# Kernel tuning notes

Hardware: AMD Instinct MI355X
Metric: run time of the kernel (lower is better)

Reference implementation:

```python
import jax, jax.numpy as jnp
import numpy as np

HIDDEN = 256
HEADS = 8
HEAD_DIM = HIDDEN // HEADS  # 32
N_NODES = 50000
N_EDGES = 800000


def setup_inputs() -> dict:
    key = jax.random.key(0)
    ks = jax.random.split(key, 12)
    h = jax.random.normal(ks[0], (N_NODES, HIDDEN), dtype=jnp.float32)
    row = jax.random.randint(ks[1], (N_EDGES,), 0, N_NODES, dtype=jnp.int64 if jax.config.jax_enable_x64 else jnp.int32)
    col = jax.random.randint(ks[2], (N_EDGES,), 0, N_NODES, dtype=jnp.int64 if jax.config.jax_enable_x64 else jnp.int32)
    def lin(kw, kb):
        W = jax.random.normal(kw, (HIDDEN, HIDDEN), dtype=jnp.float32) * 0.02
        b = jax.random.normal(kb, (HIDDEN,), dtype=jnp.float32) * 0.02
        return W, b
    Wq, bq = lin(ks[3], ks[4])
    Wk, bk = lin(ks[5], ks[6])
    Wv, bv = lin(ks[7], ks[8])
    Wo, bo = lin(ks[9], ks[10])
    return {"h": h, "row": row, "col": col,
            "Wq": Wq, "bq": bq, "Wk": Wk, "bk": bk,
            "Wv": Wv, "bv": bv, "Wo": Wo, "bo": bo}


def reference(h, row, col, Wq, bq, Wk, bk, Wv, bv, Wo, bo):
    N = h.shape[0]
    scaling = HEAD_DIM ** (-0.5)
    # torch Linear: x @ W.T + b; reshape to (N, head_dim, num_heads) as in source
    q = (h @ Wq.T + bq).reshape(N, HEAD_DIM, HEADS) * scaling
    k = (h @ Wk.T + bk).reshape(N, HEAD_DIM, HEADS)
    v = (h @ Wv.T + bv).reshape(N, HEAD_DIM, HEADS)
    # SDDMM: per-edge, per-head score = q[row] . k[col]   -> [E, H]
    s = jnp.einsum('edh,edh->eh', q[row], k[col])
    # sparse softmax over nonzeros of each row
    m = jax.ops.segment_max(s, row, num_segments=N)          # [N, H]
    e = jnp.exp(s - m[row])                                   # [E, H]
    z = jax.ops.segment_sum(e, row, num_segments=N)          # [N, H]
    attn = e / z[row]                                         # [E, H]
    # SPMM: out[i] = sum over edges (i,j) attn[e,h] * v[j,:,h]
    out = jax.ops.segment_sum(attn[:, None, :] * v[col], row, num_segments=N)  # [N, D, H]
    return out.reshape(N, -1) @ Wo.T + bo
```

## Files before the change

kernel.cpp:

```cpp
#include <hip/hip_runtime.h>
#include <hip/hip_bf16.h>
#include <math.h>

#define N_NODES  50000
#define N_EDGES  800000
#define HIDDEN   256
#define HEADS    8
#define HEAD_DIM 32
#define MAXDEG   64
#define KVSTRIDE 512
#define QKV_NB   2346
#define O_NB     782

#define PREP_BKT   391
#define PREP_HCONV 6400
#define PREP_W     450
#define PREP_NB    (PREP_BKT + PREP_HCONV + PREP_W)

using short8 = __attribute__((ext_vector_type(8))) short;
using f32x4  = __attribute__((ext_vector_type(4))) float;

__device__ __forceinline__ float b2f(unsigned short u) {
  union { unsigned int i; float f; } v; v.i = ((unsigned int)u) << 16; return v.f;
}
__device__ __forceinline__ unsigned short f2b(float f) {
  union { float f; unsigned int i; } v; v.f = f;
  unsigned int r = v.i + 0x7FFF + ((v.i >> 16) & 1);
  return (unsigned short)(r >> 16);
}
__device__ __forceinline__ void unpack2(unsigned int d, float& lo, float& hi) {
  union { unsigned int i; float f; } a, b;
  a.i = d << 16; b.i = d & 0xFFFF0000u;
  lo = a.f; hi = b.f;
}

template<int NB, int NCT>
__device__ __forceinline__ void xcd_map(int b, int& rt, int& ct) {
  constexpr int q = NB / 8, r = NB % 8;
  const int xcd = b & 7, j = b >> 3;
  const int id = (xcd < r ? xcd * (q + 1) : r * (q + 1) + (xcd - r) * q) + j;
  rt = id / NCT; ct = id - rt * NCT;
}

__global__ __launch_bounds__(256) void init(const unsigned short* __restrict__ h16,
                                            const int* __restrict__ rowraw,
                                            int* __restrict__ flags,
                                            int* __restrict__ cur) {
  const int tid = threadIdx.x;
  if (blockIdx.x == 0) {
    __shared__ int nan_cnt, hi_viol, lo_pos;
    if (tid == 0) { nan_cnt = 0; hi_viol = 0; lo_pos = 0; }
    __syncthreads();
    int local = 0;
    for (int i = tid; i < 16384; i += 256)
      if ((h16[i] & 0x7F80) == 0x7F80) local++;
    if (local) atomicAdd(&nan_cnt, local);
    int viol = 0, pos = 0;
    for (int e = tid; e < 512; e += 256) {
      if (rowraw[2 * e + 1] != 0) viol++;
      if (rowraw[2 * e] > 0) pos++;
    }
    if (viol) atomicAdd(&hi_viol, viol);
    if (pos) atomicAdd(&lo_pos, pos);
    __syncthreads();
    if (tid == 0) {
      flags[0] = (nan_cnt >= 4) ? 1 : 0;
      flags[1] = (hi_viol == 0 && lo_pos > 0) ? 1 : 0;
    }
  } else {
    const int i = (blockIdx.x - 1) * 256 + tid;
    if (i < N_NODES / 4) ((int4*)cur)[i] = make_int4(0, 0, 0, 0);
  }
}

struct WPtrs {
  const void* srcW[4]; unsigned short* dstW[4];
  const void* srcB[4]; unsigned short* dstB[4];
};

__global__ __launch_bounds__(256) void prep(
    const void* __restrict__ hsrc, unsigned short* __restrict__ Hc, WPtrs p,
    const int* __restrict__ rowraw, const int* __restrict__ colraw,
    const int* __restrict__ flags, int* __restrict__ cursor,
    unsigned short* __restrict__ bucket)
{
  const int fp32 = flags[0];
  const int bid = blockIdx.x, tid = threadIdx.x;

  if (bid < PREP_BKT) {
    const int t = bid * 256 + tid;
    if (t < N_EDGES / 8) {
      const int i64 = flags[1];
      const int e0 = t * 8;
      int r[8], c[8];
      #pragma unroll
      for (int x = 0; x < 8; ++x) {
        const int e = e0 + x;
        r[x] = i64 ? rowraw[2 * e] : rowraw[e];
        c[x] = i64 ? colraw[2 * e] : colraw[e];
      }
      int pos[8];
      #pragma unroll
      for (int x = 0; x < 8; ++x)
        pos[x] = atomicAdd(&cursor[r[x]], 1);
      #pragma unroll
      for (int x = 0; x < 8; ++x)
        if (pos[x] < MAXDEG) bucket[r[x] * MAXDEG + pos[x]] = (unsigned short)c[x];
    }
  } else if (bid < PREP_BKT + PREP_HCONV) {
    const int n4 = N_NODES * HIDDEN / 4;
    for (int i = (bid - PREP_BKT) * 256 + tid; i < n4; i += PREP_HCONV * 256) {
      if (fp32) {
        const float4 v = ((const float4*)hsrc)[i];
        ushort4 o; o.x = f2b(v.x); o.y = f2b(v.y); o.z = f2b(v.z); o.w = f2b(v.w);
        ((ushort4*)Hc)[i] = o;
      } else {
        ((ushort4*)Hc)[i] = ((const ushort4*)hsrc)[i];
      }
    }
  } else {
    const int idx = (bid - PREP_BKT - PREP_HCONV) * 256 + tid;
    if (idx < 49152) {
      const int m = idx >> 14, r = idx & 16383;
      const int g = r >> 6, kc = r & 63;
      const int f = ((g & 31) << 3) | (g >> 5);
      const int s = f * 64 + kc;
      if (fp32) {
        const float4 v = ((const float4*)p.srcW[m])[s];
        ushort4 o; o.x = f2b(v.x); o.y = f2b(v.y); o.z = f2b(v.z); o.w = f2b(v.w);
        ((ushort4*)p.dstW[m])[g * 64 + kc] = o;
      } else {
        ((ushort4*)p.dstW[m])[g * 64 + kc] = ((const ushort4*)p.srcW[m])[s];
      }
    } else if (idx < 49152 + 65536) {
      const int g = idx - 49152;
      const int f = g >> 8, kk = g & 255;
      const int s = f * 256 + (((kk & 31) << 3) | (kk >> 5));
      p.dstW[3][g] = fp32 ? f2b(((const float*)p.srcW[3])[s])
                          : ((const unsigned short*)p.srcW[3])[s];
    } else if (idx < 49152 + 65536 + 256) {
      const int t = idx - 49152 - 65536;
      const int m = t >> 6, r = t & 63;
      if (m < 3) {
        ushort4 o;
        #pragma unroll
        for (int x = 0; x < 4; ++x) {
          const int g = r * 4 + x;
          const int f = ((g & 31) << 3) | (g >> 5);
          ((unsigned short*)&o)[x] = fp32 ? f2b(((const float*)p.srcB[m])[f])
                                          : ((const unsigned short*)p.srcB[m])[f];
        }
        ((ushort4*)p.dstB[m])[r] = o;
      } else {
        if (fp32) {
          const float4 v = ((const float4*)p.srcB[3])[r];
          ushort4 o; o.x = f2b(v.x); o.y = f2b(v.y); o.z = f2b(v.z); o.w = f2b(v.w);
          ((ushort4*)p.dstB[3])[r] = o;
        } else {
          ((ushort4*)p.dstB[3])[r] = ((const ushort4*)p.srcB[3])[r];
        }
      }
    }
  }
}

#if defined(__has_builtin)
#if __has_builtin(__builtin_amdgcn_global_load_lds)
#define HAVE_GLL 1
#endif
#endif
__device__ __forceinline__ void stage_tile(
    const unsigned short* __restrict__ src, int row_base, int row_max,
    int kb, unsigned short* lds, int wave, int lane)
{
  #pragma unroll
  for (int c = 0; c < 4; ++c) {
    const int chunk = wave * 4 + c;
    const int r = chunk * 8 + (lane >> 3);
    int gr = row_base + r; if (gr > row_max) gr = row_max;
    const int scb = (lane & 7) ^ ((lane >> 3) & 7);
    const unsigned short* gp = src + (size_t)gr * HIDDEN + kb * 64 + scb * 8;
#ifdef HAVE_GLL
    __builtin_amdgcn_global_load_lds(
        (const __attribute__((address_space(1))) void*)gp,
        (__attribute__((address_space(3))) void*)(lds + chunk * 512),
        16, 0, 0);
#else
    *(short8*)(lds + chunk * 512 + lane * 8) = *(const short8*)gp;
#endif
  }
}

#define GEMM_CORE(A_SRC, AROWB, AROWM, B_SRC, BROWB, BROWM)                          \
  __shared__ unsigned short sA[2][8192], sB[2][8192];                                \
  const int wave = threadIdx.x >> 6, lane = threadIdx.x & 63;                        \
  const int lrow = lane & 15, quad = lane >> 4;                                      \
  const int wr0 = (wave & 1) * 64, wc0 = (wave >> 1) * 64;                           \
  f32x4 acc[4][4];                                                                   \
  _Pragma("unroll")                                                                  \
  for (int i = 0; i < 4; ++i)                                                        \
    _Pragma("unroll")                                                                \
    for (int j = 0; j < 4; ++j) acc[i][j] = (f32x4){0.f, 0.f, 0.f, 0.f};            \
  stage_tile(A_SRC, AROWB, AROWM, 0, sA[0], wave, lane);                             \
  stage_tile(B_SRC, BROWB, BROWM, 0, sB[0], wave, lane);                             \
  _Pragma("unroll")                                                                  \
  for (int kb = 0; kb < 4; ++kb) {                                                   \
    __syncthreads();                          \
    if (kb < 3) {                                                                    \
      stage_tile(A_SRC, AROWB, AROWM, kb + 1, sA[(kb + 1) & 1], wave, lane);         \
      stage_tile(B_SRC, BROWB, BROWM, kb + 1, sB[(kb + 1) & 1], wave, lane);         \
    }                                                                                \
    const unsigned short* pA = sA[kb & 1];                                           \
    const unsigned short* pB = sB[kb & 1];                                           \
    _Pragma("unroll")                                                                \
    for (int kk = 0; kk < 2; ++kk) {                                                 \
      short8 af[4], bf[4];                                                           \
      _Pragma("unroll")                                                              \
      for (int i = 0; i < 4; ++i) {                                                  \
        const int rr = wr0 + i * 16 + lrow;                                          \
        af[i] = *(const short8*)(pA + rr * 64 + (((kk * 4 + quad) ^ (lrow & 7)) * 8));\
      }                                                                              \
      _Pragma("unroll")                                                              \
      for (int j = 0; j < 4; ++j) {                                                  \
        const int rr = wc0 + j * 16 + lrow;                                          \
        bf[j] = *(const short8*)(pB + rr * 64 + (((kk * 4 + quad) ^ (lrow & 7)) * 8));\
      }                                                                              \
      _Pragma("unroll")                                                              \
      for (int i = 0; i < 4; ++i)                                                    \
        _Pragma("unroll")                                                            \
        for (int j = 0; j < 4; ++j)                                                  \
          acc[i][j] = __builtin_amdgcn_mfma_f32_16x16x32_bf16(af[i], bf[j], acc[i][j], 0, 0, 0); \
    }                                                                                \
  }

__global__ __launch_bounds__(256) void gemm_qkv(
    const unsigned short* __restrict__ X, const unsigned short* __restrict__ WQKV,
    const unsigned short* __restrict__ biasAll,
    unsigned short* __restrict__ Qt, unsigned short* __restrict__ KV, float qscale)
{
  int rt, ct; xcd_map<QKV_NB, 6>(blockIdx.x, rt, ct);
  const int row0 = rt * 128;
  const int col0 = ct * 128;
  GEMM_CORE(X, row0, N_NODES - 1, WQKV, col0, 767)

  #pragma unroll
  for (int j = 0; j < 4; ++j) {
    const int gcol = col0 + wc0 + j * 16;
    const int m = gcol >> 8;
    const int f = (gcol & 255) + lrow;
    const float scale = (m == 0) ? qscale : 1.0f;
    const float bv = b2f(biasAll[gcol + lrow]);
    unsigned short* bp = (m == 0) ? Qt : (KV + ((m == 2) ? 256 : 0));
    const int ldv = (m == 0) ? 256 : KVSTRIDE;
    #pragma unroll
    for (int i = 0; i < 4; ++i) {
      #pragma unroll
      for (int r = 0; r < 4; ++r) {
        const int row = row0 + wr0 + i * 16 + quad * 4 + r;
        if (row < N_NODES)
          bp[(size_t)row * ldv + f] = f2b((acc[i][j][r] + bv) * scale);
      }
    }
  }
}

__global__ __launch_bounds__(256) void gemm_o(
    const unsigned short* __restrict__ X, const unsigned short* __restrict__ W,
    const unsigned short* __restrict__ bias, void* __restrict__ Yv,
    const int* __restrict__ flags)
{
  int rt, ct; xcd_map<O_NB, 2>(blockIdx.x, rt, ct);
  const int row0 = rt * 128;
  const int col0 = ct * 128;
  const int out_fp32 = flags[0];
  GEMM_CORE(X, row0, N_NODES - 1, W, col0, 255)

  #pragma unroll
  for (int j = 0; j < 4; ++j) {
    const int col = col0 + wc0 + j * 16 + lrow;
    const float bv = b2f(bias[col]);
    #pragma unroll
    for (int i = 0; i < 4; ++i) {
      #pragma unroll
      for (int r = 0; r < 4; ++r) {
        const int row = row0 + wr0 + i * 16 + quad * 4 + r;
        if (row < N_NODES) {
          const float y = acc[i][j][r] + bv;
          if (out_fp32) ((float*)Yv)[(size_t)row * HIDDEN + col] = y;
          else ((unsigned short*)Yv)[(size_t)row * HIDDEN + col] = f2b(y);
        }
      }
    }
  }
}

__global__ __launch_bounds__(256) void attn_fused(
    const unsigned short* __restrict__ Qt, const unsigned short* __restrict__ KV,
    const int* __restrict__ cursor, const unsigned short* __restrict__ bucket,
    unsigned short* __restrict__ pre)
{
  const int node = blockIdx.x * 4 + (threadIdx.x >> 6);
  if (node >= N_NODES) return;
  const int lane = threadIdx.x & 63;
  const int side = lane >> 5;
  const int sub  = lane & 31;
  const unsigned suboff = (unsigned)(sub * 8);
  int cnt = cursor[node]; if (cnt > MAXDEG) cnt = MAXDEG;

  const uint4 qd = *(const uint4*)(Qt + (unsigned)node * HIDDEN + suboff);
  float q[8];
  unpack2(qd.x, q[0], q[1]); unpack2(qd.y, q[2], q[3]);
  unpack2(qd.z, q[4], q[5]); unpack2(qd.w, q[6], q[7]);

  float a[8] = {0.f, 0.f, 0.f, 0.f, 0.f, 0.f, 0.f, 0.f};
  float z = 0.f;

  if (cnt > 0) {
    const int last = cnt - 1;
    const unsigned short* brow = bucket + node * MAXDEG;
    const int myidx = (int)brow[lane <= last ? lane : last];
    const int nit = (cnt + 1) >> 1;

    auto compute = [&](const uint4& kk, const uint4& vv, int jj) {
      float kf[8];
      unpack2(kk.x, kf[0], kf[1]); unpack2(kk.y, kf[2], kf[3]);
      unpack2(kk.z, kf[4], kf[5]); unpack2(kk.w, kf[6], kf[7]);
      float s0 = q[0]*kf[0] + q[2]*kf[2] + q[4]*kf[4] + q[6]*kf[6];
      float s1 = q[1]*kf[1] + q[3]*kf[3] + q[5]*kf[5] + q[7]*kf[7];
      float d = s0 + s1;
      d += __shfl_xor(d, 1, 64);
      d += __shfl_xor(d, 2, 64);
      float w = __expf(d);
      if (2 * jj + side > last) w = 0.f;
      z += w;
      float vf[8];
      unpack2(vv.x, vf[0], vf[1]); unpack2(vv.y, vf[2], vf[3]);
      unpack2(vv.z, vf[4], vf[5]); unpack2(vv.w, vf[6], vf[7]);
      #pragma unroll
      for (int x = 0; x < 8; ++x) a[x] = fmaf(w, vf[x], a[x]);
    };

    const int cA = __shfl(myidx, side, 64);
    const unsigned offA = ((unsigned)cA << 9) + suboff;
    uint4 kA = *(const uint4*)(KV + offA);
    uint4 vA = *(const uint4*)(KV + offA + 256u);

    const int cB = __shfl(myidx, 2 + side, 64);
    const unsigned offB = ((unsigned)cB << 9) + suboff;
    uint4 kB = *(const uint4*)(KV + offB);
    uint4 vB = *(const uint4*)(KV + offB + 256u);

    int slC = 4 + side;
    int cC = __shfl(myidx, slC, 64);

    int j = 0;
    #pragma unroll 2
    for (; j + 2 < nit; ++j) {
      const unsigned offC = ((unsigned)cC << 9) + suboff;
      const uint4 kC = *(const uint4*)(KV + offC);
      const uint4 vC = *(const uint4*)(KV + offC + 256u);
      int sl = 2 * (j + 3) + side; if (sl > 63) sl = 63;
      cC = __shfl(myidx, sl, 64);
      compute(kA, vA, j);
      kA = kB; vA = vB; kB = kC; vB = vC;
    }
    compute(kA, vA, j);
    if (j + 1 < nit) compute(kB, vB, j + 1);
  }

  #pragma unroll
  for (int x = 0; x < 8; ++x) a[x] += __shfl_xor(a[x], 32, 64);
  z += __shfl_xor(z, 32, 64);
  const float zi = (z > 0.f) ? (1.f / z) : 0.f;

  if (side == 0) {
    short8 ov;
    #pragma unroll
    for (int x = 0; x < 8; ++x) ov[x] = (short)f2b(a[x] * zi);
    *(short8*)(pre + (unsigned)node * HIDDEN + suboff) = ov;
  }
}

extern "C" void kernel_launch(void* const* d_in, const int* in_sizes, int n_in,
                              void* d_out, int out_size, void* d_ws, size_t ws_size,
                              hipStream_t stream) {
  const void* h_raw  = d_in[0];
  const int* row_raw = (const int*)d_in[1];
  const int* col_raw = (const int*)d_in[2];
  const void* Wq_raw = d_in[3]; const void* bq_raw = d_in[4];
  const void* Wk_raw = d_in[5]; const void* bk_raw = d_in[6];
  const void* Wv_raw = d_in[7]; const void* bv_raw = d_in[8];
  const void* Wo_raw = d_in[9]; const void* bo_raw = d_in[10];

  char* ws = (char*)d_ws;
  unsigned short* Qt   = (unsigned short*)(ws +          0);
  unsigned short* KV   = (unsigned short*)(ws +  25600000);
  int*            cur  = (int*)           (ws +  76800000);
  unsigned short* bkt  = (unsigned short*)(ws +  77000000);
  unsigned short* pre  = (unsigned short*)(ws +  89800000);
  unsigned short* WqP  = (unsigned short*)(ws + 115400000);
  unsigned short* WkP  = WqP + 65536;
  unsigned short* WvP  = WkP + 65536;
  unsigned short* WoP  = WvP + 65536;
  unsigned short* bqP  = (unsigned short*)(ws + 116000000);
  unsigned short* bkP  = bqP + 256;
  unsigned short* bvP  = bkP + 256;
  unsigned short* boC  = bvP + 256;
  int*            flags = (int*)(ws + 116100000);
  unsigned short* Hc   = (unsigned short*)(ws + 117000000);

  init<<<64, 256, 0, stream>>>((const unsigned short*)h_raw, row_raw, flags, cur);

  WPtrs wp;
  wp.srcW[0] = Wq_raw; wp.srcW[1] = Wk_raw; wp.srcW[2] = Wv_raw; wp.srcW[3] = Wo_raw;
  wp.dstW[0] = WqP;    wp.dstW[1] = WkP;    wp.dstW[2] = WvP;    wp.dstW[3] = WoP;
  wp.srcB[0] = bq_raw; wp.srcB[1] = bk_raw; wp.srcB[2] = bv_raw; wp.srcB[3] = bo_raw;
  wp.dstB[0] = bqP;    wp.dstB[1] = bkP;    wp.dstB[2] = bvP;    wp.dstB[3] = boC;
  prep<<<PREP_NB, 256, 0, stream>>>(h_raw, Hc, wp, row_raw, col_raw, flags, cur, bkt);

  gemm_qkv<<<QKV_NB, 256, 0, stream>>>(Hc, WqP, bqP, Qt, KV, 0.17677669529663687f);

  attn_fused<<<(N_NODES + 3) / 4, 256, 0, stream>>>(Qt, KV, cur, bkt, pre);

  gemm_o<<<O_NB, 256, 0, stream>>>(pre, WoP, boC, d_out, flags);
}
```

Before: 359.8 us.

## Interleave edge bucketing blocks into QKV GEMM launch and parallelize dtype detection

Moves the edge-bucketing work (atomic cursor increments and bucket writes) out of the prep kernel and into the QKV GEMM launch, giving every seventh block to bucketing so the memory/atomic-bound scatter can overlap with the compute-bound GEMM blocks. The dtype-detection reduction is now spread over all init blocks with wave ballots and global atomic counters, reset by a memset, instead of one block looping over the sample. Downstream kernels derive the flags from the raw counters. This adds a memset launch and some divergent blocks inside the GEMM grid that could upset the XCD tile mapping.

```diff
diff --git a/kernel.cpp b/kernel.cpp
--- a/kernel.cpp
+++ b/kernel.cpp
@@ -11,11 +11,10 @@
 #define KVSTRIDE 512
 #define QKV_NB   2346
 #define O_NB     782
-
-#define PREP_BKT   391
+#define BKT_NB   391
+#define QKVB_NB  (QKV_NB + BKT_NB)
 #define PREP_HCONV 6400
-#define PREP_W     450
-#define PREP_NB    (PREP_BKT + PREP_HCONV + PREP_W)
+#define PREP_NB  (PREP_HCONV + 450)
 
 using short8 = __attribute__((ext_vector_type(8))) short;
 using f32x4  = __attribute__((ext_vector_type(4))) float;
@@ -33,6 +32,9 @@
   a.i = d << 16; b.i = d & 0xFFFF0000u;
   lo = a.f; hi = b.f;
 }
+
+__device__ __forceinline__ int flag_fp32(const int* cnt) { return cnt[0] >= 4; }
+__device__ __forceinline__ int flag_i64 (const int* cnt) { return cnt[1] == 0 && cnt[2] > 0; }
 
 template<int NB, int NCT>
 __device__ __forceinline__ void xcd_map(int b, int& rt, int& ct) {
@@ -44,32 +46,25 @@
 
 __global__ __launch_bounds__(256) void init(const unsigned short* __restrict__ h16,
                                             const int* __restrict__ rowraw,
-                                            int* __restrict__ flags,
+                                            int* __restrict__ cnt,
                                             int* __restrict__ cur) {
-  const int tid = threadIdx.x;
-  if (blockIdx.x == 0) {
-    __shared__ int nan_cnt, hi_viol, lo_pos;
-    if (tid == 0) { nan_cnt = 0; hi_viol = 0; lo_pos = 0; }
-    __syncthreads();
-    int local = 0;
-    for (int i = tid; i < 16384; i += 256)
-      if ((h16[i] & 0x7F80) == 0x7F80) local++;
-    if (local) atomicAdd(&nan_cnt, local);
+  const int tid = threadIdx.x, bid = blockIdx.x;
+  const int i = bid * 256 + tid;
+  const int isnan16 = (h16[i] & 0x7F80) == 0x7F80;
+  const unsigned long long m = __ballot(isnan16);
+  if ((tid & 63) == 0 && m) atomicAdd(&cnt[0], __popcll(m));
+
+  if (bid == 0) {
     int viol = 0, pos = 0;
     for (int e = tid; e < 512; e += 256) {
       if (rowraw[2 * e + 1] != 0) viol++;
       if (rowraw[2 * e] > 0) pos++;
     }
-    if (viol) atomicAdd(&hi_viol, viol);
-    if (pos) atomicAdd(&lo_pos, pos);
-    __syncthreads();
-    if (tid == 0) {
-      flags[0] = (nan_cnt >= 4) ? 1 : 0;
-      flags[1] = (hi_viol == 0 && lo_pos > 0) ? 1 : 0;
-    }
+    if (viol) atomicAdd(&cnt[1], viol);
+    if (pos) atomicAdd(&cnt[2], pos);
   } else {
-    const int i = (blockIdx.x - 1) * 256 + tid;
-    if (i < N_NODES / 4) ((int4*)cur)[i] = make_int4(0, 0, 0, 0);
+    const int j = (bid - 1) * 256 + tid;
+    if (j < N_NODES / 4) ((int4*)cur)[j] = make_int4(0, 0, 0, 0);
   }
 }
 
@@ -80,36 +75,14 @@
 
 __global__ __launch_bounds__(256) void prep(
     const void* __restrict__ hsrc, unsigned short* __restrict__ Hc, WPtrs p,
-    const int* __restrict__ rowraw, const int* __restrict__ colraw,
-    const int* __restrict__ flags, int* __restrict__ cursor,
-    unsigned short* __restrict__ bucket)
+    const int* __restrict__ cnt)
 {
-  const int fp32 = flags[0];
+  const int fp32 = flag_fp32(cnt);
   const int bid = blockIdx.x, tid = threadIdx.x;
 
-  if (bid < PREP_BKT) {
-    const int t = bid * 256 + tid;
-    if (t < N_EDGES / 8) {
-      const int i64 = flags[1];
-      const int e0 = t * 8;
-      int r[8], c[8];
-      #pragma unroll
-      for (int x = 0; x < 8; ++x) {
-        const int e = e0 + x;
-        r[x] = i64 ? rowraw[2 * e] : rowraw[e];
-        c[x] = i64 ? colraw[2 * e] : colraw[e];
-      }
-      int pos[8];
-      #pragma unroll
-      for (int x = 0; x < 8; ++x)
-        pos[x] = atomicAdd(&cursor[r[x]], 1);
-      #pragma unroll
-      for (int x = 0; x < 8; ++x)
-        if (pos[x] < MAXDEG) bucket[r[x] * MAXDEG + pos[x]] = (unsigned short)c[x];
-    }
-  } else if (bid < PREP_BKT + PREP_HCONV) {
+  if (bid < PREP_HCONV) {
     const int n4 = N_NODES * HIDDEN / 4;
-    for (int i = (bid - PREP_BKT) * 256 + tid; i < n4; i += PREP_HCONV * 256) {
+    for (int i = bid * 256 + tid; i < n4; i += PREP_HCONV * 256) {
       if (fp32) {
         const float4 v = ((const float4*)hsrc)[i];
         ushort4 o; o.x = f2b(v.x); o.y = f2b(v.y); o.z = f2b(v.z); o.w = f2b(v.w);
@@ -119,7 +92,7 @@
       }
     }
   } else {
-    const int idx = (bid - PREP_BKT - PREP_HCONV) * 256 + tid;
+    const int idx = (bid - PREP_HCONV) * 256 + tid;
     if (idx < 49152) {
       const int m = idx >> 14, r = idx & 16383;
       const int g = r >> 6, kc = r & 63;
@@ -236,9 +209,36 @@
 __global__ __launch_bounds__(256) void gemm_qkv(
     const unsigned short* __restrict__ X, const unsigned short* __restrict__ WQKV,
     const unsigned short* __restrict__ biasAll,
-    unsigned short* __restrict__ Qt, unsigned short* __restrict__ KV, float qscale)
+    unsigned short* __restrict__ Qt, unsigned short* __restrict__ KV, float qscale,
+    const int* __restrict__ rowraw, const int* __restrict__ colraw,
+    const int* __restrict__ cnt, int* __restrict__ cursor,
+    unsigned short* __restrict__ bucket)
 {
-  int rt, ct; xcd_map<QKV_NB, 6>(blockIdx.x, rt, ct);
+  const int b = blockIdx.x;
+  if (b % 7 == 6) {
+    const int t = (b / 7) * 256 + threadIdx.x;
+    if (t < N_EDGES / 8) {
+      const int i64 = flag_i64(cnt);
+      const int e0 = t * 8;
+      int r[8], c[8];
+      #pragma unroll
+      for (int x = 0; x < 8; ++x) {
+        const int e = e0 + x;
+        r[x] = i64 ? rowraw[2 * e] : rowraw[e];
+        c[x] = i64 ? colraw[2 * e] : colraw[e];
+      }
+      int pos[8];
+      #pragma unroll
+      for (int x = 0; x < 8; ++x)
+        pos[x] = atomicAdd(&cursor[r[x]], 1);
+      #pragma unroll
+      for (int x = 0; x < 8; ++x)
+        if (pos[x] < MAXDEG) bucket[r[x] * MAXDEG + pos[x]] = (unsigned short)c[x];
+    }
+    return;
+  }
+  const int gid = b - (b + 1) / 7;
+  int rt, ct; xcd_map<QKV_NB, 6>(gid, rt, ct);
   const int row0 = rt * 128;
   const int col0 = ct * 128;
   GEMM_CORE(X, row0, N_NODES - 1, WQKV, col0, 767)
@@ -267,12 +267,12 @@
 __global__ __launch_bounds__(256) void gemm_o(
     const unsigned short* __restrict__ X, const unsigned short* __restrict__ W,
     const unsigned short* __restrict__ bias, void* __restrict__ Yv,
-    const int* __restrict__ flags)
+    const int* __restrict__ cnt)
 {
   int rt, ct; xcd_map<O_NB, 2>(blockIdx.x, rt, ct);
   const int row0 = rt * 128;
   const int col0 = ct * 128;
-  const int out_fp32 = flags[0];
+  const int out_fp32 = flag_fp32(cnt);
   GEMM_CORE(X, row0, N_NODES - 1, W, col0, 255)
 
   #pragma unroll
@@ -406,21 +406,23 @@
   unsigned short* bkP  = bqP + 256;
   unsigned short* bvP  = bkP + 256;
   unsigned short* boC  = bvP + 256;
-  int*            flags = (int*)(ws + 116100000);
+  int*            cnt  = (int*)(ws + 116100000);
   unsigned short* Hc   = (unsigned short*)(ws + 117000000);
 
-  init<<<64, 256, 0, stream>>>((const unsigned short*)h_raw, row_raw, flags, cur);
+  hipMemsetAsync(cnt, 0, 16, stream);
+  init<<<64, 256, 0, stream>>>((const unsigned short*)h_raw, row_raw, cnt, cur);
 
   WPtrs wp;
   wp.srcW[0] = Wq_raw; wp.srcW[1] = Wk_raw; wp.srcW[2] = Wv_raw; wp.srcW[3] = Wo_raw;
   wp.dstW[0] = WqP;    wp.dstW[1] = WkP;    wp.dstW[2] = WvP;    wp.dstW[3] = WoP;
   wp.srcB[0] = bq_raw; wp.srcB[1] = bk_raw; wp.srcB[2] = bv_raw; wp.srcB[3] = bo_raw;
   wp.dstB[0] = bqP;    wp.dstB[1] = bkP;    wp.dstB[2] = bvP;    wp.dstB[3] = boC;
-  prep<<<PREP_NB, 256, 0, stream>>>(h_raw, Hc, wp, row_raw, col_raw, flags, cur, bkt);
-
-  gemm_qkv<<<QKV_NB, 256, 0, stream>>>(Hc, WqP, bqP, Qt, KV, 0.17677669529663687f);
+  prep<<<PREP_NB, 256, 0, stream>>>(h_raw, Hc, wp, cnt);
+
+  gemm_qkv<<<QKVB_NB, 256, 0, stream>>>(Hc, WqP, bqP, Qt, KV, 0.17677669529663687f,
+                                        row_raw, col_raw, cnt, cur, bkt);
 
   attn_fused<<<(N_NODES + 3) / 4, 256, 0, stream>>>(Qt, KV, cur, bkt, pre);
 
-  gemm_o<<<O_NB, 256, 0, stream>>>(pre, WoP, boC, d_out, flags);
-}
+  gemm_o<<<O_NB, 256, 0, stream>>>(pre, WoP, boC, d_out, cnt);
+}
```

Result: faster. 347.2 us (-3.5%).
